# Optimization experiments

Measured on AMD Instinct MI355X. Metric: run time of the kernel, lower is better.

Reference implementation:

```python
import jax, jax.numpy as jnp
import numpy as np

N, C, NIRR, E = 2048, 128, 9, 10          # nodes, channels, sum(2l+1) of input irreps, num elements
DOUT = (1, 3)                              # output irrep dims for 128x0e + 128x1o
K3, K2, K1 = 4, 3, 2                       # number of CG paths per correlation order


def setup_inputs() -> dict:
    key = jax.random.key(0)
    ks = jax.random.split(key, 24)
    inp = {
        'node_feats': jax.random.normal(ks[0], (N, C, NIRR), jnp.float32),
        'node_attrs': jax.nn.one_hot(jax.random.randint(ks[1], (N,), 0, E), E, dtype=jnp.float32),
        'sc': jax.random.normal(ks[2], (N, C * sum(DOUT)), jnp.float32),
    }
    i = 3
    for li, d in enumerate(DOUT):
        # U tensors: fixed (buffer) generalized CG coupling tensors; sparse in e3nn,
        # here random dense stand-ins with the exact same shapes / contraction structure.
        inp[f'u3_l{li}'] = 0.1 * jax.random.normal(ks[i + 0], (d, NIRR, NIRR, NIRR, K3), jnp.float32)
        inp[f'u2_l{li}'] = 0.1 * jax.random.normal(ks[i + 1], (d, NIRR, NIRR, K2), jnp.float32)
        inp[f'u1_l{li}'] = 0.1 * jax.random.normal(ks[i + 2], (d, NIRR, K1), jnp.float32)
        s3, s2, s1 = 1.0 / np.sqrt(K3 * C), 1.0 / np.sqrt(K2 * C), 1.0 / np.sqrt(K1 * C)
        inp[f'w3_l{li}'] = s3 * jax.random.normal(ks[i + 3], (E, K3, C), jnp.float32)
        inp[f'w2_l{li}'] = s2 * jax.random.normal(ks[i + 4], (E, K2, C), jnp.float32)
        inp[f'w1_l{li}'] = s1 * jax.random.normal(ks[i + 5], (E, K1, C), jnp.float32)
        i += 6
    inp['lin_w0'] = jax.random.normal(ks[i], (C, C), jnp.float32)
    inp['lin_w1'] = jax.random.normal(ks[i + 1], (C, C), jnp.float32)
    return inp


def _contraction(x, y, u3, u2, u1, w3, w2, w1):
    # MACE Contraction: correlation-3 nested CG contraction for one output irrep.
    # x: [N,C,n], y: [N,E] one-hot, u_nu: [d, n*nu, k_nu], w_nu: [E, k_nu, C]
    wk3 = jnp.einsum('ekc,be->bkc', w3, y)                       # per-node path weights
    out = jnp.einsum('dpqik,bkc,bci->bcdpq', u3, wk3, x)         # main, nu=3
    out = jnp.einsum('dpik,ekc,be->bcdpi', u2, w2, y) + out      # add nu=2 weights
    out = jnp.einsum('bcdpi,bci->bcdp', out, x)                  # contract one feature index
    out = jnp.einsum('dik,ekc,be->bcdi', u1, w1, y) + out        # add nu=1 weights
    out = jnp.einsum('bcdi,bci->bcd', out, x)                    # [N,C,d]
    return out


def reference(node_feats, node_attrs, sc,
              u3_l0, u2_l0, u1_l0, w3_l0, w2_l0, w1_l0,
              u3_l1, u2_l1, u1_l1, w3_l1, w2_l1, w1_l1,
              lin_w0, lin_w1):
    f0 = _contraction(node_feats, node_attrs, u3_l0, u2_l0, u1_l0, w3_l0, w2_l0, w1_l0)  # [N,C,1]
    f1 = _contraction(node_feats, node_attrs, u3_l1, u2_l1, u1_l1, w3_l1, w2_l1, w1_l1)  # [N,C,3]
    inv_sqrt_c = 1.0 / np.sqrt(C).astype(np.float32)
    # o3.Linear: block-diagonal channel mixing per irrep, 1/sqrt(fan_in) normalization
    o0 = jnp.einsum('bim,ij->bjm', f0, lin_w0) * inv_sqrt_c
    o1 = jnp.einsum('bim,ij->bjm', f1, lin_w1) * inv_sqrt_c
    out = jnp.concatenate([o0.reshape(o0.shape[0], -1), o1.reshape(o1.shape[0], -1)], axis=-1)
    return out + sc
```

## Files before the change

kernel.cpp:

```cpp
#include <hip/hip_runtime.h>

#define N_NODES 2048
#define C_CH    128
#define NIRR    9
#define E_EL    10

#define NKT 14
#define UTAB_HALVES (NKT * 512)

typedef _Float16 f16x8 __attribute__((ext_vector_type(8)));
typedef float   f32x16 __attribute__((ext_vector_type(16)));
typedef float   f32x4u __attribute__((ext_vector_type(4), aligned(4)));
typedef float   pf2    __attribute__((ext_vector_type(2)));

struct MonoTab {
    unsigned char a[224], b2[224], c[224], msk[224];
};
constexpr MonoTab makeMono() {
    MonoTab m{};
    int s3 = 0;
    for (int p = 0; p < 9; p++)
        for (int q = p; q < 9; q++)
            for (int i = q; i < 9; i++) { m.a[s3] = p; m.b2[s3] = q; m.c[s3] = i; m.msk[s3] = 1; s3++; }
    int s2 = 0;
    for (int p = 0; p < 9; p++)
        for (int q = p; q < 9; q++) { m.a[165 + s2] = p; m.b2[165 + s2] = q; m.c[165 + s2] = 9; m.msk[165 + s2] = 1; s2++; }
    for (int p = 0; p < 9; p++) { m.a[210 + p] = p; m.b2[210 + p] = 9; m.c[210 + p] = 9; m.msk[210 + p] = 1; }
    for (int k = 219; k < 224; k++) { m.a[k] = 9; m.b2[k] = 9; m.c[k] = 9; m.msk[k] = 0; }
    return m;
}
constexpr MonoTab MT = makeMono();

__global__ __launch_bounds__(256) void build_utab_kernel(
    const float* __restrict__ u3_l0, const float* __restrict__ u2_l0, const float* __restrict__ u1_l0,
    const float* __restrict__ u3_l1, const float* __restrict__ u2_l1, const float* __restrict__ u1_l1,
    _Float16* __restrict__ Utab, float* __restrict__ us1f)
{
    int t = blockIdx.x * 256 + threadIdx.x;
    if (t < UTAB_HALVES) {
        int kt = t / 512, idx = t % 512;
        int lane = idx >> 3, j = idx & 7;
        int m = lane & 31, g = lane >> 5;
        int k = kt * 16 + g * 8 + j;
        float v = 0.f;
        if (m < 16) {
            int ds = m >> 2, kk = m & 3;
            if (k < 165) {
                int pp = 0, qq = 0, ii = 0, cnt = 0;
                for (int p = 0; p < 9; p++)
                    for (int q = p; q < 9; q++)
                        for (int i = q; i < 9; i++) {
                            if (cnt == k) { pp = p; qq = q; ii = i; }
                            cnt++;
                        }
                const float* u = (ds == 0) ? u3_l0 : (u3_l1 + (ds - 1) * 2916);
                int perm[6][3] = {{pp,qq,ii},{pp,ii,qq},{qq,pp,ii},{qq,ii,pp},{ii,pp,qq},{ii,qq,pp}};
                float acc = 0.f;
                #pragma unroll
                for (int w = 0; w < 6; w++)
                    acc += u[((perm[w][0] * 9 + perm[w][1]) * 9 + perm[w][2]) * 4 + kk];
                float mult = (pp == qq && qq == ii) ? 6.f : ((pp == qq || qq == ii) ? 2.f : 1.f);
                v = acc / mult;
            }
        } else if (m < 28) {
            int r = m - 16, ds = r / 3, kk = r % 3;
            if (k >= 165 && k < 210) {
                int s = k - 165;
                int pp = 0, qq = 0, cnt = 0;
                for (int p = 0; p < 9; p++)
                    for (int q = p; q < 9; q++) {
                        if (cnt == s) { pp = p; qq = q; }
                        cnt++;
                    }
                const float* u = (ds == 0) ? u2_l0 : (u2_l1 + (ds - 1) * 243);
                float acc = u[(pp * 9 + qq) * 3 + kk] + u[(qq * 9 + pp) * 3 + kk];
                v = (pp == qq) ? acc * 0.5f : acc;
            }
        } else {
            int r = m - 28, ds = r >> 1, kk = r & 1;
            if (k >= 210 && k < 219) {
                int p = k - 210;
                v = (ds == 0) ? u1_l0[p * 2 + kk] : u1_l1[(0 * 9 + p) * 2 + kk];
            }
        }
        Utab[t] = (_Float16)v;
    } else if (t < UTAB_HALVES + 72) {
        int q = t - UTAB_HALVES;
        int ds = q / 18, rem = q % 18, p = rem >> 1, kk = rem & 1;
        us1f[q] = (ds == 0) ? u1_l0[p * 2 + kk] : u1_l1[((ds - 1) * 9 + p) * 2 + kk];
    }
}

__global__ __launch_bounds__(256, 2) void fused_kernel(
    const float* __restrict__ x, const float* __restrict__ y,
    const _Float16* __restrict__ Utab, const float* __restrict__ us1f,
    const float* __restrict__ w3_l0, const float* __restrict__ w2_l0, const float* __restrict__ w1_l0,
    const float* __restrict__ w3_l1, const float* __restrict__ w2_l1, const float* __restrict__ w1_l1,
    const float* __restrict__ lw0, const float* __restrict__ lw1,
    const float* __restrict__ sc, float* __restrict__ out)
{
    __shared__ float Gbuf[256][34];
    __shared__ float fs[2][4][132];
    int tid = threadIdx.x;
    int lane = tid & 63;
    int wid = tid >> 6;
    int n = lane & 31, g = lane >> 5;
    int b0 = blockIdx.x * 2;

    const f16x8* U8 = (const f16x8*)Utab;

    #pragma unroll 1
    for (int tl = 0; tl < 2; tl++) {
        int tile = wid * 2 + tl;
        int col = tile * 32 + n;
        int node = col >> 7, c = col & 127;
        const float* xp = x + ((size_t)(b0 + node) * C_CH + c) * NIRR;
        f32x4u xa = *(const f32x4u*)xp;
        f32x4u xb = *(const f32x4u*)(xp + 4);
        float xv10[10] = {xa[0], xa[1], xa[2], xa[3], xb[0], xb[1], xb[2], xb[3], xp[8], 1.f};

        f32x16 acc;
        #pragma unroll
        for (int z = 0; z < 16; z++) acc[z] = 0.f;

        #pragma unroll
        for (int kt = 0; kt < NKT; kt++) {
            f16x8 af = U8[kt * 64 + lane];
            float mf[8];
            if (g == 0) {
                #pragma unroll
                for (int j = 0; j < 8; j++) {
                    const int k = kt * 16 + j;
                    mf[j] = MT.msk[k] ? xv10[MT.a[k]] * xv10[MT.b2[k]] * xv10[MT.c[k]] : 0.f;
                }
            } else {
                #pragma unroll
                for (int j = 0; j < 8; j++) {
                    const int k = kt * 16 + 8 + j;
                    mf[j] = MT.msk[k] ? xv10[MT.a[k]] * xv10[MT.b2[k]] * xv10[MT.c[k]] : 0.f;
                }
            }
            f16x8 bf;
            #pragma unroll
            for (int j = 0; j < 8; j++) bf[j] = (_Float16)mf[j];
            acc = __builtin_amdgcn_mfma_f32_32x32x16_f16(af, bf, acc, 0, 0, 0);
        }

        #pragma unroll
        for (int reg = 0; reg < 16; reg++) {
            int row = (reg & 3) + 8 * (reg >> 2) + 4 * g;
            Gbuf[col][row] = acc[reg];
        }
    }
    __syncthreads();

    {
        int col = tid;
        int node = col >> 7, c = col & 127;
        int b = b0 + node;
        int e = 0;
        #pragma unroll
        for (int k = 1; k < E_EL; k++)
            if (y[b * E_EL + k] > 0.5f) e = k;
        e = __builtin_amdgcn_readfirstlane(e);

        float G[32];
        #pragma unroll
        for (int row = 0; row < 32; row++) G[row] = Gbuf[col][row];

        const float* xp = x + ((size_t)b * C_CH + c) * NIRR;
        f32x4u xa = *(const f32x4u*)xp;
        f32x4u xb = *(const f32x4u*)(xp + 4);
        float xvp[9] = {xa[0], xa[1], xa[2], xa[3], xb[0], xb[1], xb[2], xb[3], xp[8]};

        float G1hi[4];
        #pragma unroll
        for (int dd = 0; dd < 2; dd++) {
            #pragma unroll
            for (int kk = 0; kk < 2; kk++) {
                float a = 0.f;
                #pragma unroll
                for (int p = 0; p < 9; p++)
                    a += us1f[(2 + dd) * 18 + p * 2 + kk] * xvp[p];
                G1hi[dd * 2 + kk] = a;
            }
        }

        {
            float acc0 = 0.f;
            #pragma unroll
            for (int kk = 0; kk < 4; kk++) acc0 += w3_l0[(e * 4 + kk) * 128 + c] * G[kk];
            #pragma unroll
            for (int kk = 0; kk < 3; kk++) acc0 += w2_l0[(e * 3 + kk) * 128 + c] * G[16 + kk];
            #pragma unroll
            for (int kk = 0; kk < 2; kk++) acc0 += w1_l0[(e * 2 + kk) * 128 + c] * G[28 + kk];
            fs[node][0][c] = acc0;
        }
        #pragma unroll
        for (int ds = 1; ds < 4; ds++) {
            float a = 0.f;
            #pragma unroll
            for (int kk = 0; kk < 4; kk++) a += w3_l1[(e * 4 + kk) * 128 + c] * G[ds * 4 + kk];
            #pragma unroll
            for (int kk = 0; kk < 3; kk++) a += w2_l1[(e * 3 + kk) * 128 + c] * G[16 + ds * 3 + kk];
            #pragma unroll
            for (int kk = 0; kk < 2; kk++) {
                float g1 = (ds < 2) ? G[28 + ds * 2 + kk] : G1hi[(ds - 2) * 2 + kk];
                a += w1_l1[(e * 2 + kk) * 128 + c] * g1;
            }
            fs[node][ds][c] = a;
        }
    }
    __syncthreads();

    {
        int nn = tid >> 7;
        int t = tid & 127;
        int b = b0 + nn;
        int sel, m = 0, j0;
        const float4* W4;
        bool isl0 = (t < 32);
        if (isl0) { sel = 0; j0 = 4 * t; W4 = (const float4*)lw0; }
        else {
            int idx = t - 32;
            m = idx >> 5;
            j0 = 4 * (idx & 31);
            sel = 1 + m;
            W4 = (const float4*)lw1;
        }
        int wbase = j0 >> 2;

        pf2 ap01 = {0.f, 0.f}, ap23 = {0.f, 0.f};
        #pragma unroll 4
        for (int ib = 0; ib < 32; ib++) {
            float4 f = *(const float4*)&fs[nn][sel][4 * ib];
            float fr[4] = {f.x, f.y, f.z, f.w};
            #pragma unroll
            for (int r = 0; r < 4; r++) {
                float4 w = W4[(4 * ib + r) * 32 + wbase];
                pf2 wlo = {w.x, w.y};
                pf2 whi = {w.z, w.w};
                pf2 fsp = {fr[r], fr[r]};
                ap01 = __builtin_elementwise_fma(wlo, fsp, ap01);
                ap23 = __builtin_elementwise_fma(whi, fsp, ap23);
            }
        }
        float a0 = ap01[0], a1 = ap01[1], a2 = ap23[0], a3 = ap23[1];

        const float inv_sqrt_c = 0.08838834764831845f;
        if (isl0) {
            size_t o = (size_t)b * 512 + j0;
            float4 s = *(const float4*)(sc + o);
            float4 rr;
            rr.x = a0 * inv_sqrt_c + s.x;
            rr.y = a1 * inv_sqrt_c + s.y;
            rr.z = a2 * inv_sqrt_c + s.z;
            rr.w = a3 * inv_sqrt_c + s.w;
            *(float4*)(out + o) = rr;
        } else {
            float av[4] = {a0, a1, a2, a3};
            #pragma unroll
            for (int jj = 0; jj < 4; jj++) {
                size_t o = (size_t)b * 512 + 128 + 3 * (j0 + jj) + m;
                out[o] = av[jj] * inv_sqrt_c + sc[o];
            }
        }
    }
}

extern "C" void kernel_launch(void* const* d_in, const int* in_sizes, int n_in,
                              void* d_out, int out_size, void* d_ws, size_t ws_size,
                              hipStream_t stream) {
    const float* x     = (const float*)d_in[0];
    const float* y     = (const float*)d_in[1];
    const float* sc    = (const float*)d_in[2];
    const float* u3_l0 = (const float*)d_in[3];
    const float* u2_l0 = (const float*)d_in[4];
    const float* u1_l0 = (const float*)d_in[5];
    const float* w3_l0 = (const float*)d_in[6];
    const float* w2_l0 = (const float*)d_in[7];
    const float* w1_l0 = (const float*)d_in[8];
    const float* u3_l1 = (const float*)d_in[9];
    const float* u2_l1 = (const float*)d_in[10];
    const float* u1_l1 = (const float*)d_in[11];
    const float* w3_l1 = (const float*)d_in[12];
    const float* w2_l1 = (const float*)d_in[13];
    const float* w1_l1 = (const float*)d_in[14];
    const float* lw0   = (const float*)d_in[15];
    const float* lw1   = (const float*)d_in[16];
    float* out = (float*)d_out;

    _Float16* Utab = (_Float16*)d_ws;
    float* us1f = (float*)((char*)d_ws + UTAB_HALVES * 2);

    build_utab_kernel<<<(UTAB_HALVES + 72 + 255) / 256, 256, 0, stream>>>(
        u3_l0, u2_l0, u1_l0, u3_l1, u2_l1, u1_l1, Utab, us1f);
    fused_kernel<<<N_NODES / 2, 256, 0, stream>>>(
        x, y, Utab, us1f,
        w3_l0, w2_l0, w1_l0, w3_l1, w2_l1, w1_l1,
        lw0, lw1, sc, out);
}
```

Measured before the change: 122.1 us.

## Process four nodes per block, one wave per node, shuffle-transpose MFMA output

Each block now handles four nodes with one wave per node. The MFMA accumulator halves are exchanged with a cross-half lane shuffle instead of round-tripping through a large LDS G buffer, which removes one barrier and the second x reload. The final linear stage computes two nodes per thread, so each loaded weight float4 is reused twice. In exchange, half the lanes do redundant epilogue work (only g==0 writes), register pressure goes up, and the grid is halved.

New measurement: 116.0 us. -5.0%, faster.

```diff
diff --git a/kernel.cpp b/kernel.cpp
--- a/kernel.cpp
+++ b/kernel.cpp
@@ -99,22 +99,26 @@
     const float* __restrict__ lw0, const float* __restrict__ lw1,
     const float* __restrict__ sc, float* __restrict__ out)
 {
-    __shared__ float Gbuf[256][34];
-    __shared__ float fs[2][4][132];
+    __shared__ float fs[4][4][132];
     int tid = threadIdx.x;
     int lane = tid & 63;
     int wid = tid >> 6;
     int n = lane & 31, g = lane >> 5;
-    int b0 = blockIdx.x * 2;
+    int b0 = blockIdx.x * 4;
+    int b = b0 + wid;
 
     const f16x8* U8 = (const f16x8*)Utab;
 
+    int e = 0;
+    #pragma unroll
+    for (int k = 1; k < E_EL; k++)
+        if (y[b * E_EL + k] > 0.5f) e = k;
+    e = __builtin_amdgcn_readfirstlane(e);
+
     #pragma unroll 1
-    for (int tl = 0; tl < 2; tl++) {
-        int tile = wid * 2 + tl;
-        int col = tile * 32 + n;
-        int node = col >> 7, c = col & 127;
-        const float* xp = x + ((size_t)(b0 + node) * C_CH + c) * NIRR;
+    for (int tl = 0; tl < 4; tl++) {
+        int c = tl * 32 + n;
+        const float* xp = x + ((size_t)b * C_CH + c) * NIRR;
         f32x4u xa = *(const f32x4u*)xp;
         f32x4u xb = *(const f32x4u*)(xp + 4);
         float xv10[10] = {xa[0], xa[1], xa[2], xa[3], xb[0], xb[1], xb[2], xb[3], xp[8], 1.f};
@@ -146,32 +150,15 @@
             acc = __builtin_amdgcn_mfma_f32_32x32x16_f16(af, bf, acc, 0, 0, 0);
         }
 
+        float G[32];
         #pragma unroll
         for (int reg = 0; reg < 16; reg++) {
-            int row = (reg & 3) + 8 * (reg >> 2) + 4 * g;
-            Gbuf[col][row] = acc[reg];
-        }
-    }
-    __syncthreads();
-
-    {
-        int col = tid;
-        int node = col >> 7, c = col & 127;
-        int b = b0 + node;
-        int e = 0;
-        #pragma unroll
-        for (int k = 1; k < E_EL; k++)
-            if (y[b * E_EL + k] > 0.5f) e = k;
-        e = __builtin_amdgcn_readfirstlane(e);
-
-        float G[32];
-        #pragma unroll
-        for (int row = 0; row < 32; row++) G[row] = Gbuf[col][row];
-
-        const float* xp = x + ((size_t)b * C_CH + c) * NIRR;
-        f32x4u xa = *(const f32x4u*)xp;
-        f32x4u xb = *(const f32x4u*)(xp + 4);
-        float xvp[9] = {xa[0], xa[1], xa[2], xa[3], xb[0], xb[1], xb[2], xb[3], xp[8]};
+            float own = acc[reg];
+            float oth = __shfl_xor(own, 32, 64);
+            int base = (reg & 3) + 8 * (reg >> 2);
+            G[base]     = (g == 0) ? own : oth;
+            G[base + 4] = (g == 0) ? oth : own;
+        }
 
         float G1hi[4];
         #pragma unroll
@@ -181,21 +168,23 @@
                 float a = 0.f;
                 #pragma unroll
                 for (int p = 0; p < 9; p++)
-                    a += us1f[(2 + dd) * 18 + p * 2 + kk] * xvp[p];
+                    a += us1f[(2 + dd) * 18 + p * 2 + kk] * xv10[p];
                 G1hi[dd * 2 + kk] = a;
             }
         }
 
+        float f0;
         {
-            float acc0 = 0.f;
-            #pragma unroll
-            for (int kk = 0; kk < 4; kk++) acc0 += w3_l0[(e * 4 + kk) * 128 + c] * G[kk];
-            #pragma unroll
-            for (int kk = 0; kk < 3; kk++) acc0 += w2_l0[(e * 3 + kk) * 128 + c] * G[16 + kk];
-            #pragma unroll
-            for (int kk = 0; kk < 2; kk++) acc0 += w1_l0[(e * 2 + kk) * 128 + c] * G[28 + kk];
-            fs[node][0][c] = acc0;
-        }
+            float a = 0.f;
+            #pragma unroll
+            for (int kk = 0; kk < 4; kk++) a += w3_l0[(e * 4 + kk) * 128 + c] * G[kk];
+            #pragma unroll
+            for (int kk = 0; kk < 3; kk++) a += w2_l0[(e * 3 + kk) * 128 + c] * G[16 + kk];
+            #pragma unroll
+            for (int kk = 0; kk < 2; kk++) a += w1_l0[(e * 2 + kk) * 128 + c] * G[28 + kk];
+            f0 = a;
+        }
+        float f123[3];
         #pragma unroll
         for (int ds = 1; ds < 4; ds++) {
             float a = 0.f;
@@ -208,15 +197,20 @@
                 float g1 = (ds < 2) ? G[28 + ds * 2 + kk] : G1hi[(ds - 2) * 2 + kk];
                 a += w1_l1[(e * 2 + kk) * 128 + c] * g1;
             }
-            fs[node][ds][c] = a;
+            f123[ds - 1] = a;
+        }
+        if (g == 0) {
+            fs[wid][0][c] = f0;
+            fs[wid][1][c] = f123[0];
+            fs[wid][2][c] = f123[1];
+            fs[wid][3][c] = f123[2];
         }
     }
     __syncthreads();
 
     {
-        int nn = tid >> 7;
+        int p = tid >> 7;
         int t = tid & 127;
-        int b = b0 + nn;
         int sel, m = 0, j0;
         const float4* W4;
         bool isl0 = (t < 32);
@@ -230,39 +224,69 @@
         }
         int wbase = j0 >> 2;
 
-        pf2 ap01 = {0.f, 0.f}, ap23 = {0.f, 0.f};
+        pf2 a01A = {0.f, 0.f}, a23A = {0.f, 0.f};
+        pf2 a01B = {0.f, 0.f}, a23B = {0.f, 0.f};
         #pragma unroll 4
         for (int ib = 0; ib < 32; ib++) {
-            float4 f = *(const float4*)&fs[nn][sel][4 * ib];
-            float fr[4] = {f.x, f.y, f.z, f.w};
+            float4 fA = *(const float4*)&fs[p][sel][4 * ib];
+            float4 fB = *(const float4*)&fs[p + 2][sel][4 * ib];
+            float frA[4] = {fA.x, fA.y, fA.z, fA.w};
+            float frB[4] = {fB.x, fB.y, fB.z, fB.w};
             #pragma unroll
             for (int r = 0; r < 4; r++) {
                 float4 w = W4[(4 * ib + r) * 32 + wbase];
                 pf2 wlo = {w.x, w.y};
                 pf2 whi = {w.z, w.w};
-                pf2 fsp = {fr[r], fr[r]};
-                ap01 = __builtin_elementwise_fma(wlo, fsp, ap01);
-                ap23 = __builtin_elementwise_fma(whi, fsp, ap23);
-            }
-        }
-        float a0 = ap01[0], a1 = ap01[1], a2 = ap23[0], a3 = ap23[1];
-
+                pf2 fra = {frA[r], frA[r]};
+                pf2 frb = {frB[r], frB[r]};
+                a01A = __builtin_elementwise_fma(wlo, fra, a01A);
+                a23A = __builtin_elementwise_fma(whi, fra, a23A);
+                a01B = __builtin_elementwise_fma(wlo, frb, a01B);
+                a23B = __builtin_elementwise_fma(whi, frb, a23B);
+            }
+        }
         const float inv_sqrt_c = 0.08838834764831845f;
-        if (isl0) {
-            size_t o = (size_t)b * 512 + j0;
-            float4 s = *(const float4*)(sc + o);
-            float4 rr;
-            rr.x = a0 * inv_sqrt_c + s.x;
-            rr.y = a1 * inv_sqrt_c + s.y;
-            rr.z = a2 * inv_sqrt_c + s.z;
-            rr.w = a3 * inv_sqrt_c + s.w;
-            *(float4*)(out + o) = rr;
-        } else {
-            float av[4] = {a0, a1, a2, a3};
-            #pragma unroll
-            for (int jj = 0; jj < 4; jj++) {
-                size_t o = (size_t)b * 512 + 128 + 3 * (j0 + jj) + m;
-                out[o] = av[jj] * inv_sqrt_c + sc[o];
+
+        {
+            int bb = b0 + p;
+            float a0 = a01A[0], a1 = a01A[1], a2 = a23A[0], a3 = a23A[1];
+            if (isl0) {
+                size_t o = (size_t)bb * 512 + j0;
+                float4 s = *(const float4*)(sc + o);
+                float4 rr;
+                rr.x = a0 * inv_sqrt_c + s.x;
+                rr.y = a1 * inv_sqrt_c + s.y;
+                rr.z = a2 * inv_sqrt_c + s.z;
+                rr.w = a3 * inv_sqrt_c + s.w;
+                *(float4*)(out + o) = rr;
+            } else {
+                float av[4] = {a0, a1, a2, a3};
+                #pragma unroll
+                for (int jj = 0; jj < 4; jj++) {
+                    size_t o = (size_t)bb * 512 + 128 + 3 * (j0 + jj) + m;
+                    out[o] = av[jj] * inv_sqrt_c + sc[o];
+                }
+            }
+        }
+        {
+            int bb = b0 + p + 2;
+            float a0 = a01B[0], a1 = a01B[1], a2 = a23B[0], a3 = a23B[1];
+            if (isl0) {
+                size_t o = (size_t)bb * 512 + j0;
+                float4 s = *(const float4*)(sc + o);
+                float4 rr;
+                rr.x = a0 * inv_sqrt_c + s.x;
+                rr.y = a1 * inv_sqrt_c + s.y;
+                rr.z = a2 * inv_sqrt_c + s.z;
+                rr.w = a3 * inv_sqrt_c + s.w;
+                *(float4*)(out + o) = rr;
+            } else {
+                float av[4] = {a0, a1, a2, a3};
+                #pragma unroll
+                for (int jj = 0; jj < 4; jj++) {
+                    size_t o = (size_t)bb * 512 + 128 + 3 * (j0 + jj) + m;
+                    out[o] = av[jj] * inv_sqrt_c + sc[o];
+                }
             }
         }
     }
@@ -295,7 +319,7 @@
 
     build_utab_kernel<<<(UTAB_HALVES + 72 + 255) / 256, 256, 0, stream>>>(
         u3_l0, u2_l0, u1_l0, u3_l1, u2_l1, u1_l1, Utab, us1f);
-    fused_kernel<<<N_NODES / 2, 256, 0, stream>>>(
+    fused_kernel<<<N_NODES / 4, 256, 0, stream>>>(
         x, y, Utab, us1f,
         w3_l0, w2_l0, w1_l0, w3_l1, w2_l1, w1_l1,
         lw0, lw1, sc, out);
```
